# Performance work log

Measured on AMD Instinct MI355X. Metric: run time of the kernel, lower is better.

The kernel has to match this reference:

```python
import jax, jax.numpy as jnp
import numpy as np

B, T, I, H, O, L = 64, 2048, 128, 256, 1, 2


def _lstm_layer(x, w_ih, w_hh, b_ih, b_hh):
    # x: [B, T, in]; w_ih: [4H, in]; w_hh: [4H, H]; biases: [4H]
    # Batch the input-side GEMM across all timesteps (torch gate order: i, f, g, o)
    xg = jnp.einsum('bti,gi->btg', x, w_ih) + b_ih + b_hh  # [B, T, 4H]
    h0 = jnp.zeros((x.shape[0], w_hh.shape[1]), x.dtype)
    c0 = jnp.zeros_like(h0)

    def step(carry, xt):
        h, c = carry
        g = xt + h @ w_hh.T  # [B, 4H]
        i, f, gg, o = jnp.split(g, 4, axis=-1)
        i = jax.nn.sigmoid(i)
        f = jax.nn.sigmoid(f)
        gg = jnp.tanh(gg)
        o = jax.nn.sigmoid(o)
        c = f * c + i * gg
        h = o * jnp.tanh(c)
        return (h, c), h

    _, hs = jax.lax.scan(step, (h0, c0), jnp.swapaxes(xg, 0, 1))  # [T, B, H]
    return jnp.swapaxes(hs, 0, 1)  # [B, T, H]


def setup_inputs() -> dict:
    key = jax.random.key(0)
    ks = jax.random.split(key, 11)
    s_i = 1.0 / np.sqrt(H)
    return {
        'x': jax.random.normal(ks[0], (B, T, I), jnp.float32),
        'w_ih0': jax.random.uniform(ks[1], (4 * H, I), jnp.float32, -s_i, s_i),
        'w_hh0': jax.random.uniform(ks[2], (4 * H, H), jnp.float32, -s_i, s_i),
        'b_ih0': jax.random.uniform(ks[3], (4 * H,), jnp.float32, -s_i, s_i),
        'b_hh0': jax.random.uniform(ks[4], (4 * H,), jnp.float32, -s_i, s_i),
        'w_ih1': jax.random.uniform(ks[5], (4 * H, H), jnp.float32, -s_i, s_i),
        'w_hh1': jax.random.uniform(ks[6], (4 * H, H), jnp.float32, -s_i, s_i),
        'b_ih1': jax.random.uniform(ks[7], (4 * H,), jnp.float32, -s_i, s_i),
        'b_hh1': jax.random.uniform(ks[8], (4 * H,), jnp.float32, -s_i, s_i),
        'fc_w': jax.random.uniform(ks[9], (O, H), jnp.float32, -s_i, s_i),
        'fc_b': jax.random.uniform(ks[10], (O,), jnp.float32, -s_i, s_i),
    }


def reference(x, w_ih0, w_hh0, b_ih0, b_hh0, w_ih1, w_hh1, b_ih1, b_hh1, fc_w, fc_b):
    h = _lstm_layer(x, w_ih0, w_hh0, b_ih0, b_hh0)
    h = _lstm_layer(h, w_ih1, w_hh1, b_ih1, b_hh1)
    h = jax.nn.relu(h)            # relu on full sequence output (as in source)
    last = h[:, -1, :]            # [B, H]
    return last @ fc_w.T + fc_b   # [B, O]
```

## Files before the change

### kernel.cpp

```cpp
#include <hip/hip_runtime.h>

#define NT 2048
#define NI 128
#define NH 256
#define WPG 32
#define BPG 8

typedef unsigned long long u64;

__device__ __forceinline__ float sigm(float v) {
  return 1.0f / (1.0f + __expf(-v));
}
__device__ __forceinline__ float tanh_fast(float v) {
  v = fminf(fmaxf(v, -15.0f), 15.0f);
  float e = __expf(-2.0f * v);
  return (1.0f - e) / (1.0f + e);
}
__device__ __forceinline__ float lstm_act(float gi, float gf, float gg, float go,
                                          float& c) {
  const float ii = sigm(gi), ff = sigm(gf), gt = tanh_fast(gg), oo = sigm(go);
  c = ff * c + ii * gt;
  return oo * tanh_fast(c);
}

__device__ __forceinline__ int ld_flag(const int* p) {
  return __hip_atomic_load(p, __ATOMIC_RELAXED, __HIP_MEMORY_SCOPE_AGENT);
}
__device__ __forceinline__ void st_flag(int* p, int v) {
  __hip_atomic_store(p, v, __ATOMIC_RELAXED, __HIP_MEMORY_SCOPE_AGENT);
}
__device__ __forceinline__ void st_h(float* p, float v) {
  __hip_atomic_store(p, v, __ATOMIC_RELAXED, __HIP_MEMORY_SCOPE_AGENT);
}
__device__ __forceinline__ u64 ld_h64(const u64* p) {
  return __hip_atomic_load(p, __ATOMIC_RELAXED, __HIP_MEMORY_SCOPE_AGENT);
}

template <int CTRL>
__device__ __forceinline__ float dppadd(float x) {
  int s = __builtin_amdgcn_update_dpp(0, __float_as_int(x), CTRL, 0xf, 0xf, true);
  return x + __int_as_float(s);
}
__device__ __forceinline__ float red16(float v) {
  v = dppadd<0xB1>(v);
  v = dppadd<0x4E>(v);
  v = dppadd<0x141>(v);
  v = dppadd<0x140>(v);
  return v;
}

__global__ __launch_bounds__(512, 1) void lstm_persistent(
    const float* __restrict__ x,
    const float* __restrict__ wih0, const float* __restrict__ whh0,
    const float* __restrict__ bih0, const float* __restrict__ bhh0,
    const float* __restrict__ wih1, const float* __restrict__ whh1,
    const float* __restrict__ bih1, const float* __restrict__ bhh1,
    const float* __restrict__ fcw, const float* __restrict__ fcb,
    float* __restrict__ out,
    float* __restrict__ h0buf, float* __restrict__ h1buf,
    int* __restrict__ flags)
{
  extern __shared__ float sm[];
  float* zz = sm;

  const int tid = threadIdx.x;
  const int bid = blockIdx.x;
  const int g = bid & 7;
  const int j = bid >> 3;
  const int b0 = g * BPG;
  int* fA = flags + g * WPG;
  int* fB = flags + 256 + g * WPG;

  const bool isL0 = (tid < 256);
  const int lane = tid & 63;
  const int wv = (tid & 255) >> 6;
  const int ks = lane & 15;
  const int rg2 = (lane >> 4) & 1;
  const int bg = lane >> 5;
  const int u = wv * 2 + rg2;
  const int col = j * 8 + u;

  float w[4][32];
  float bs[4];
  if (isL0) {
#pragma unroll
    for (int gt = 0; gt < 4; ++gt) {
      const int R = gt * NH + col;
      bs[gt] = bih0[R] + bhh0[R];
#pragma unroll
      for (int c = 0; c < 6; ++c)
#pragma unroll
        for (int e = 0; e < 4; ++e) {
          const int k = ks * 4 + 64 * c + e;
          w[gt][c * 4 + e] = (k < NI) ? wih0[R * NI + k] : whh0[R * NH + (k - NI)];
        }
    }
  } else {
#pragma unroll
    for (int gt = 0; gt < 4; ++gt) {
      const int R = gt * NH + col;
      bs[gt] = bih1[R] + bhh1[R];
#pragma unroll
      for (int c = 0; c < 8; ++c)
#pragma unroll
        for (int e = 0; e < 4; ++e) {
          const int k = ks * 4 + 64 * c + e;
          w[gt][c * 4 + e] = (k < NH) ? wih1[R * NH + k] : whh1[R * NH + (k - NH)];
        }
    }
  }

  float cellA0 = 0.f, cellA1 = 0.f, cellB0 = 0.f, cellB1 = 0.f;
  u64 rh0 = 0, rh1 = 0;
  float4 xv = make_float4(0.f, 0.f, 0.f, 0.f);
  if (tid < 128) {
    xv = *reinterpret_cast<const float4*>(
        x + (size_t)(b0 + (tid >> 5)) * NT * NI + (tid & 31) * 4);
  }
  __syncthreads();

#pragma unroll 1
  for (int it = 0; it <= NT; ++it) {
#pragma unroll
    for (int half = 0; half < 2; ++half) {
      const int xb = half ? 4 : 0;
      int* fSelf = half ? fB : fA;
      int* fOther = half ? fA : fB;
      const int nit = half ? it + 1 : it;
      const int oxb = half ? 0 : 4;

      if (tid < 128 && it < NT)
        *reinterpret_cast<float4*>(&zz[(tid >> 5) * 640 + (tid & 31) * 4]) = xv;
      *reinterpret_cast<u64*>(&zz[(tid >> 7) * 640 + 128 + (tid & 127) * 2]) = rh0;
      *reinterpret_cast<u64*>(&zz[(tid >> 7) * 640 + 384 + (tid & 127) * 2]) = rh1;
      __syncthreads();

      if (isL0) {
        if (it < NT) {
          float acc[4][2] = {{0.f, 0.f}, {0.f, 0.f}, {0.f, 0.f}, {0.f, 0.f}};
          const float* z0 = &zz[(bg * 2 + 0) * 640 + ks * 4];
          const float* z1 = &zz[(bg * 2 + 1) * 640 + ks * 4];
#pragma unroll
          for (int c = 0; c < 6; ++c) {
            const float4 v0 = *reinterpret_cast<const float4*>(z0 + 64 * c);
            const float4 v1 = *reinterpret_cast<const float4*>(z1 + 64 * c);
#pragma unroll
            for (int gt = 0; gt < 4; ++gt) {
              acc[gt][0] = fmaf(w[gt][c * 4 + 0], v0.x, acc[gt][0]);
              acc[gt][0] = fmaf(w[gt][c * 4 + 1], v0.y, acc[gt][0]);
              acc[gt][0] = fmaf(w[gt][c * 4 + 2], v0.z, acc[gt][0]);
              acc[gt][0] = fmaf(w[gt][c * 4 + 3], v0.w, acc[gt][0]);
              acc[gt][1] = fmaf(w[gt][c * 4 + 0], v1.x, acc[gt][1]);
              acc[gt][1] = fmaf(w[gt][c * 4 + 1], v1.y, acc[gt][1]);
              acc[gt][1] = fmaf(w[gt][c * 4 + 2], v1.z, acc[gt][1]);
              acc[gt][1] = fmaf(w[gt][c * 4 + 3], v1.w, acc[gt][1]);
            }
          }
#pragma unroll
          for (int gt = 0; gt < 4; ++gt) {
            acc[gt][0] = red16(acc[gt][0]);
            acc[gt][1] = red16(acc[gt][1]);
          }
          float ca = half ? cellB0 : cellA0;
          const float ha = lstm_act(acc[0][0] + bs[0], acc[1][0] + bs[1],
                                    acc[2][0] + bs[2], acc[3][0] + bs[3], ca);
          if (half) cellB0 = ca; else cellA0 = ca;
          float cb = half ? cellB1 : cellA1;
          const float hb = lstm_act(acc[0][1] + bs[0], acc[1][1] + bs[1],
                                    acc[2][1] + bs[2], acc[3][1] + bs[3], cb);
          if (half) cellB1 = cb; else cellA1 = cb;
          if ((lane & 15) == 0) {
            const size_t base = (size_t)(it & 1) * 64;
            st_h(&h0buf[(base + (b0 + xb + bg * 2 + 0)) * NH + col], ha);
            st_h(&h0buf[(base + (b0 + xb + bg * 2 + 1)) * NH + col], hb);
          }
        }
      } else {
        if (it >= 1) {
          float acc[4][2] = {{0.f, 0.f}, {0.f, 0.f}, {0.f, 0.f}, {0.f, 0.f}};
          const float* z0 = &zz[(bg * 2 + 0) * 640 + 128 + ks * 4];
          const float* z1 = &zz[(bg * 2 + 1) * 640 + 128 + ks * 4];
#pragma unroll
          for (int c = 0; c < 8; ++c) {
            const float4 v0 = *reinterpret_cast<const float4*>(z0 + 64 * c);
            const float4 v1 = *reinterpret_cast<const float4*>(z1 + 64 * c);
#pragma unroll
            for (int gt = 0; gt < 4; ++gt) {
              acc[gt][0] = fmaf(w[gt][c * 4 + 0], v0.x, acc[gt][0]);
              acc[gt][0] = fmaf(w[gt][c * 4 + 1], v0.y, acc[gt][0]);
              acc[gt][0] = fmaf(w[gt][c * 4 + 2], v0.z, acc[gt][0]);
              acc[gt][0] = fmaf(w[gt][c * 4 + 3], v0.w, acc[gt][0]);
              acc[gt][1] = fmaf(w[gt][c * 4 + 0], v1.x, acc[gt][1]);
              acc[gt][1] = fmaf(w[gt][c * 4 + 1], v1.y, acc[gt][1]);
              acc[gt][1] = fmaf(w[gt][c * 4 + 2], v1.z, acc[gt][1]);
              acc[gt][1] = fmaf(w[gt][c * 4 + 3], v1.w, acc[gt][1]);
            }
          }
#pragma unroll
          for (int gt = 0; gt < 4; ++gt) {
            acc[gt][0] = red16(acc[gt][0]);
            acc[gt][1] = red16(acc[gt][1]);
          }
          float ca = half ? cellB0 : cellA0;
          const float ha = lstm_act(acc[0][0] + bs[0], acc[1][0] + bs[1],
                                    acc[2][0] + bs[2], acc[3][0] + bs[3], ca);
          if (half) cellB0 = ca; else cellA0 = ca;
          float cb = half ? cellB1 : cellA1;
          const float hb = lstm_act(acc[0][1] + bs[0], acc[1][1] + bs[1],
                                    acc[2][1] + bs[2], acc[3][1] + bs[3], cb);
          if (half) cellB1 = cb; else cellA1 = cb;
          if ((lane & 15) == 0) {
            const size_t base = (size_t)((it - 1) & 1) * 64;
            st_h(&h1buf[(base + (b0 + xb + bg * 2 + 0)) * NH + col], ha);
            st_h(&h1buf[(base + (b0 + xb + bg * 2 + 1)) * NH + col], hb);
          }
        }
      }

      if (tid < WPG) {
        int guard = 0;
        while (ld_flag(&fOther[tid]) < nit) {
          __builtin_amdgcn_s_sleep(1);
          if (++guard > 100000000) break;
        }
      }
      __syncthreads();

      if (nit <= NT) {
        const int p0 = (nit - 1) & 1;
        const int p1 = nit & 1;
        const int bl = tid >> 7, off = (tid & 127) * 2;
        rh0 = ld_h64(reinterpret_cast<const u64*>(
            h0buf + ((size_t)p0 * 64 + (b0 + oxb + bl)) * NH + off));
        rh1 = ld_h64(reinterpret_cast<const u64*>(
            h1buf + ((size_t)p1 * 64 + (b0 + oxb + bl)) * NH + off));
        if (tid < 128 && nit < NT) {
          xv = *reinterpret_cast<const float4*>(
              x + ((size_t)(b0 + oxb + (tid >> 5)) * NT + (size_t)nit) * NI +
              (tid & 31) * 4);
        }
      }

      if (nit <= NT) {
        if (tid < 128 && nit < NT)
          asm volatile("s_waitcnt vmcnt(3)" ::: "memory");
        else
          asm volatile("s_waitcnt vmcnt(2)" ::: "memory");
      } else {
        asm volatile("s_waitcnt vmcnt(0)" ::: "memory");
      }
      __builtin_amdgcn_s_barrier();
      if (tid == 0) st_flag(&fSelf[j], it + 1);
    }
  }

  if (j == 0) {
    if (tid < WPG) {
      int guard = 0;
      while (ld_flag(&fA[tid]) < NT + 1 || ld_flag(&fB[tid]) < NT + 1) {
        __builtin_amdgcn_s_sleep(1);
        if (++guard > 100000000) break;
      }
    }
    __syncthreads();
    const int bb = tid >> 6, ln = tid & 63;
    const float* hrow = h1buf + ((size_t)(((NT - 1) & 1)) * 64 + (b0 + bb)) * NH;
    const u64 u0 = ld_h64(reinterpret_cast<const u64*>(hrow + ln * 4));
    const u64 u1 = ld_h64(reinterpret_cast<const u64*>(hrow + ln * 4 + 2));
    const float ha = __uint_as_float((unsigned)u0);
    const float hb = __uint_as_float((unsigned)(u0 >> 32));
    const float hc = __uint_as_float((unsigned)u1);
    const float hd = __uint_as_float((unsigned)(u1 >> 32));
    const float4 w4 = *reinterpret_cast<const float4*>(fcw + ln * 4);
    float p = fmaxf(ha, 0.f) * w4.x + fmaxf(hb, 0.f) * w4.y +
              fmaxf(hc, 0.f) * w4.z + fmaxf(hd, 0.f) * w4.w;
#pragma unroll
    for (int off = 32; off >= 1; off >>= 1) p += __shfl_down(p, off, 64);
    if (ln == 0) out[b0 + bb] = p + fcb[0];
  }
}

extern "C" void kernel_launch(void* const* d_in, const int* in_sizes, int n_in,
                              void* d_out, int out_size, void* d_ws, size_t ws_size,
                              hipStream_t stream) {
  (void)in_sizes; (void)n_in; (void)out_size; (void)ws_size;
  const float* x    = (const float*)d_in[0];
  const float* wih0 = (const float*)d_in[1];
  const float* whh0 = (const float*)d_in[2];
  const float* bih0 = (const float*)d_in[3];
  const float* bhh0 = (const float*)d_in[4];
  const float* wih1 = (const float*)d_in[5];
  const float* whh1 = (const float*)d_in[6];
  const float* bih1 = (const float*)d_in[7];
  const float* bhh1 = (const float*)d_in[8];
  const float* fcw  = (const float*)d_in[9];
  const float* fcb  = (const float*)d_in[10];
  float* out = (float*)d_out;

  float* ws = (float*)d_ws;
  float* h0buf = ws;
  float* h1buf = ws + 2 * 64 * 256;
  int* flags = (int*)(ws + 4 * 64 * 256);

  const size_t zbytes = (size_t)(4 * 64 * 256) * sizeof(float) + 512 * sizeof(int);
  hipMemsetAsync(d_ws, 0, zbytes, stream);

  size_t shmem = 96 * 1024;
  if (hipFuncSetAttribute(reinterpret_cast<const void*>(lstm_persistent),
                          hipFuncAttributeMaxDynamicSharedMemorySize,
                          (int)shmem) != hipSuccess) {
    shmem = 2560 * sizeof(float);
  }

  hipLaunchKernelGGL(lstm_persistent, dim3(256), dim3(512), shmem, stream,
                     x, wih0, whh0, bih0, bhh0, wih1, whh1, bih1, bhh1,
                     fcw, fcb, out, h0buf, h1buf, flags);
}
```

Baseline: 10.74 ms.

## Restructure LSTM step sync: per-wave flag polling, gathered h stores, blocked h layout

Rewrites the per-half-step schedule of the persistent LSTM kernel. Each wave now spins on the other half's flags itself, so the extra block barrier is gone and the h/x prefetch is issued before the matvec rather than after it. Each lane computes a single batch element's activation, and the h values are gathered in shared memory. One wave then writes them as 64-bit stores and publishes the flag, using a new blocked h-buffer layout (group, column-block, batch) with padded shared rows (ZROW=644) to cut bank conflicts. This is meant to shorten the critical path of each recurrent step, at the cost of more complex indexing and a single writer wave that serialises the flag publish.

```diff
diff --git a/kernel.cpp b/kernel.cpp
--- a/kernel.cpp
+++ b/kernel.cpp
@@ -5,6 +5,7 @@
 #define NH 256
 #define WPG 32
 #define BPG 8
+#define ZROW 644
 
 typedef unsigned long long u64;
 
@@ -29,11 +30,11 @@
 __device__ __forceinline__ void st_flag(int* p, int v) {
   __hip_atomic_store(p, v, __ATOMIC_RELAXED, __HIP_MEMORY_SCOPE_AGENT);
 }
-__device__ __forceinline__ void st_h(float* p, float v) {
-  __hip_atomic_store(p, v, __ATOMIC_RELAXED, __HIP_MEMORY_SCOPE_AGENT);
-}
 __device__ __forceinline__ u64 ld_h64(const u64* p) {
   return __hip_atomic_load(p, __ATOMIC_RELAXED, __HIP_MEMORY_SCOPE_AGENT);
+}
+__device__ __forceinline__ void st_h64(u64* p, u64 v) {
+  __hip_atomic_store(p, v, __ATOMIC_RELAXED, __HIP_MEMORY_SCOPE_AGENT);
 }
 
 template <int CTRL>
@@ -61,7 +62,8 @@
     int* __restrict__ flags)
 {
   extern __shared__ float sm[];
-  float* zz = sm;
+  float* zz  = sm;
+  float* gat = sm + 4 * ZROW;
 
   const int tid = threadIdx.x;
   const int bid = blockIdx.x;
@@ -79,6 +81,8 @@
   const int bg = lane >> 5;
   const int u = wv * 2 + rg2;
   const int col = j * 8 + u;
+  const int sel = ks & 1;
+  const int myb = bg * 2 + sel;
 
   float w[4][32];
   float bs[4];
@@ -110,13 +114,20 @@
     }
   }
 
-  float cellA0 = 0.f, cellA1 = 0.f, cellB0 = 0.f, cellB1 = 0.f;
+  const int pj = tid >> 4;
+  const int pr = tid & 15;
+  const int pb = pr >> 2;
+  const int pu = pr & 3;
+  const int stage_h0 = pb * ZROW + 128 + pj * 8 + pu * 2;
+  const int stage_h1 = pb * ZROW + 384 + pj * 8 + pu * 2;
+  const int pre_base = (g * 32 + pj) * 64 + pb * 8 + pu * 2;
+  const float* xA = x + (size_t)(b0 + 0 + (tid >> 5)) * NT * NI + (tid & 31) * 4;
+  const float* xB = x + (size_t)(b0 + 4 + (tid >> 5)) * NT * NI + (tid & 31) * 4;
+
+  float cA = 0.f, cB = 0.f;
   u64 rh0 = 0, rh1 = 0;
   float4 xv = make_float4(0.f, 0.f, 0.f, 0.f);
-  if (tid < 128) {
-    xv = *reinterpret_cast<const float4*>(
-        x + (size_t)(b0 + (tid >> 5)) * NT * NI + (tid & 31) * 4);
-  }
+  if (tid < 128) xv = *reinterpret_cast<const float4*>(xA);
   __syncthreads();
 
 #pragma unroll 1
@@ -130,18 +141,39 @@
       const int oxb = half ? 0 : 4;
 
       if (tid < 128 && it < NT)
-        *reinterpret_cast<float4*>(&zz[(tid >> 5) * 640 + (tid & 31) * 4]) = xv;
-      *reinterpret_cast<u64*>(&zz[(tid >> 7) * 640 + 128 + (tid & 127) * 2]) = rh0;
-      *reinterpret_cast<u64*>(&zz[(tid >> 7) * 640 + 384 + (tid & 127) * 2]) = rh1;
+        *reinterpret_cast<float4*>(&zz[(tid >> 5) * ZROW + (tid & 31) * 4]) = xv;
+      *reinterpret_cast<u64*>(&zz[stage_h0]) = rh0;
+      *reinterpret_cast<u64*>(&zz[stage_h1]) = rh1;
       __syncthreads();
 
-      if (isL0) {
-        if (it < NT) {
-          float acc[4][2] = {{0.f, 0.f}, {0.f, 0.f}, {0.f, 0.f}, {0.f, 0.f}};
-          const float* z0 = &zz[(bg * 2 + 0) * 640 + ks * 4];
-          const float* z1 = &zz[(bg * 2 + 1) * 640 + ks * 4];
-#pragma unroll
-          for (int c = 0; c < 6; ++c) {
+      if (nit <= NT) {
+        if (lane < WPG) {
+          int guard = 0;
+          while (ld_flag(&fOther[lane]) < nit) {
+            __builtin_amdgcn_s_sleep(1);
+            if (++guard > 50000000) break;
+          }
+        }
+        asm volatile("" ::: "memory");
+        const int o0 = ((nit - 1) & 1) * 16384 + oxb * 8 + pre_base;
+        const int o1 = (nit & 1) * 16384 + oxb * 8 + pre_base;
+        rh0 = ld_h64(reinterpret_cast<const u64*>(h0buf + o0));
+        rh1 = ld_h64(reinterpret_cast<const u64*>(h1buf + o1));
+        if (tid < 128 && nit < NT) {
+          xv = *reinterpret_cast<const float4*>((half ? xA : xB) +
+                                                (size_t)nit * NI);
+        }
+      }
+
+      if (isL0 ? (it < NT) : (it >= 1)) {
+        float acc[4][2] = {{0.f, 0.f}, {0.f, 0.f}, {0.f, 0.f}, {0.f, 0.f}};
+        const int koff = isL0 ? (ks * 4) : (128 + ks * 4);
+        const float* z0 = &zz[(bg * 2 + 0) * ZROW + koff];
+        const float* z1 = &zz[(bg * 2 + 1) * ZROW + koff];
+        const int NC = isL0 ? 6 : 8;
+#pragma unroll
+        for (int c = 0; c < 8; ++c) {
+          if (c < NC) {
             const float4 v0 = *reinterpret_cast<const float4*>(z0 + 64 * c);
             const float4 v1 = *reinterpret_cast<const float4*>(z1 + 64 * c);
 #pragma unroll
@@ -156,101 +188,40 @@
               acc[gt][1] = fmaf(w[gt][c * 4 + 3], v1.w, acc[gt][1]);
             }
           }
-#pragma unroll
-          for (int gt = 0; gt < 4; ++gt) {
-            acc[gt][0] = red16(acc[gt][0]);
-            acc[gt][1] = red16(acc[gt][1]);
+        }
+        float s0[4];
+#pragma unroll
+        for (int gt = 0; gt < 4; ++gt) {
+          const float ra = red16(acc[gt][0]);
+          const float rb = red16(acc[gt][1]);
+          s0[gt] = (sel ? rb : ra) + bs[gt];
+        }
+        float c = half ? cB : cA;
+        const float h = lstm_act(s0[0], s0[1], s0[2], s0[3], c);
+        if (half) cB = c; else cA = c;
+        if (ks < 2) gat[(isL0 ? 0 : 32) + myb * 8 + u] = h;
+      }
+      asm volatile("s_waitcnt lgkmcnt(0)" ::: "memory");
+      __builtin_amdgcn_s_barrier();
+
+      if ((tid >> 6) == 1) {
+        const int l = tid & 63;
+        if (l < 32) {
+          const int layer = l >> 4, l4 = l & 15;
+          const bool ok = layer ? (it >= 1) : (it < NT);
+          if (ok) {
+            const int par = layer ? ((it - 1) & 1) : (it & 1);
+            float* hb = layer ? h1buf : h0buf;
+            const u64 v = *reinterpret_cast<const u64*>(
+                &gat[layer * 32 + (l4 >> 2) * 8 + (l4 & 3) * 2]);
+            st_h64(reinterpret_cast<u64*>(hb + par * 16384 + (g * 32 + j) * 64 +
+                                          (xb + (l4 >> 2)) * 8 + (l4 & 3) * 2),
+                   v);
           }
-          float ca = half ? cellB0 : cellA0;
-          const float ha = lstm_act(acc[0][0] + bs[0], acc[1][0] + bs[1],
-                                    acc[2][0] + bs[2], acc[3][0] + bs[3], ca);
-          if (half) cellB0 = ca; else cellA0 = ca;
-          float cb = half ? cellB1 : cellA1;
-          const float hb = lstm_act(acc[0][1] + bs[0], acc[1][1] + bs[1],
-                                    acc[2][1] + bs[2], acc[3][1] + bs[3], cb);
-          if (half) cellB1 = cb; else cellA1 = cb;
-          if ((lane & 15) == 0) {
-            const size_t base = (size_t)(it & 1) * 64;
-            st_h(&h0buf[(base + (b0 + xb + bg * 2 + 0)) * NH + col], ha);
-            st_h(&h0buf[(base + (b0 + xb + bg * 2 + 1)) * NH + col], hb);
-          }
-        }
-      } else {
-        if (it >= 1) {
-          float acc[4][2] = {{0.f, 0.f}, {0.f, 0.f}, {0.f, 0.f}, {0.f, 0.f}};
-          const float* z0 = &zz[(bg * 2 + 0) * 640 + 128 + ks * 4];
-          const float* z1 = &zz[(bg * 2 + 1) * 640 + 128 + ks * 4];
-#pragma unroll
-          for (int c = 0; c < 8; ++c) {
-            const float4 v0 = *reinterpret_cast<const float4*>(z0 + 64 * c);
-            const float4 v1 = *reinterpret_cast<const float4*>(z1 + 64 * c);
-#pragma unroll
-            for (int gt = 0; gt < 4; ++gt) {
-              acc[gt][0] = fmaf(w[gt][c * 4 + 0], v0.x, acc[gt][0]);
-              acc[gt][0] = fmaf(w[gt][c * 4 + 1], v0.y, acc[gt][0]);
-              acc[gt][0] = fmaf(w[gt][c * 4 + 2], v0.z, acc[gt][0]);
-              acc[gt][0] = fmaf(w[gt][c * 4 + 3], v0.w, acc[gt][0]);
-              acc[gt][1] = fmaf(w[gt][c * 4 + 0], v1.x, acc[gt][1]);
-              acc[gt][1] = fmaf(w[gt][c * 4 + 1], v1.y, acc[gt][1]);
-              acc[gt][1] = fmaf(w[gt][c * 4 + 2], v1.z, acc[gt][1]);
-              acc[gt][1] = fmaf(w[gt][c * 4 + 3], v1.w, acc[gt][1]);
-            }
-          }
-#pragma unroll
-          for (int gt = 0; gt < 4; ++gt) {
-            acc[gt][0] = red16(acc[gt][0]);
-            acc[gt][1] = red16(acc[gt][1]);
-          }
-          float ca = half ? cellB0 : cellA0;
-          const float ha = lstm_act(acc[0][0] + bs[0], acc[1][0] + bs[1],
-                                    acc[2][0] + bs[2], acc[3][0] + bs[3], ca);
-          if (half) cellB0 = ca; else cellA0 = ca;
-          float cb = half ? cellB1 : cellA1;
-          const float hb = lstm_act(acc[0][1] + bs[0], acc[1][1] + bs[1],
-                                    acc[2][1] + bs[2], acc[3][1] + bs[3], cb);
-          if (half) cellB1 = cb; else cellA1 = cb;
-          if ((lane & 15) == 0) {
-            const size_t base = (size_t)((it - 1) & 1) * 64;
-            st_h(&h1buf[(base + (b0 + xb + bg * 2 + 0)) * NH + col], ha);
-            st_h(&h1buf[(base + (b0 + xb + bg * 2 + 1)) * NH + col], hb);
-          }
-        }
-      }
-
-      if (tid < WPG) {
-        int guard = 0;
-        while (ld_flag(&fOther[tid]) < nit) {
-          __builtin_amdgcn_s_sleep(1);
-          if (++guard > 100000000) break;
-        }
-      }
-      __syncthreads();
-
-      if (nit <= NT) {
-        const int p0 = (nit - 1) & 1;
-        const int p1 = nit & 1;
-        const int bl = tid >> 7, off = (tid & 127) * 2;
-        rh0 = ld_h64(reinterpret_cast<const u64*>(
-            h0buf + ((size_t)p0 * 64 + (b0 + oxb + bl)) * NH + off));
-        rh1 = ld_h64(reinterpret_cast<const u64*>(
-            h1buf + ((size_t)p1 * 64 + (b0 + oxb + bl)) * NH + off));
-        if (tid < 128 && nit < NT) {
-          xv = *reinterpret_cast<const float4*>(
-              x + ((size_t)(b0 + oxb + (tid >> 5)) * NT + (size_t)nit) * NI +
-              (tid & 31) * 4);
-        }
-      }
-
-      if (nit <= NT) {
-        if (tid < 128 && nit < NT)
-          asm volatile("s_waitcnt vmcnt(3)" ::: "memory");
-        else
-          asm volatile("s_waitcnt vmcnt(2)" ::: "memory");
-      } else {
+        }
         asm volatile("s_waitcnt vmcnt(0)" ::: "memory");
-      }
-      __builtin_amdgcn_s_barrier();
-      if (tid == 0) st_flag(&fSelf[j], it + 1);
+        if ((tid & 63) == 0) st_flag(&fSelf[j], it + 1);
+      }
     }
   }
 
@@ -259,14 +230,16 @@
       int guard = 0;
       while (ld_flag(&fA[tid]) < NT + 1 || ld_flag(&fB[tid]) < NT + 1) {
         __builtin_amdgcn_s_sleep(1);
-        if (++guard > 100000000) break;
+        if (++guard > 50000000) break;
       }
     }
     __syncthreads();
     const int bb = tid >> 6, ln = tid & 63;
-    const float* hrow = h1buf + ((size_t)(((NT - 1) & 1)) * 64 + (b0 + bb)) * NH;
-    const u64 u0 = ld_h64(reinterpret_cast<const u64*>(hrow + ln * 4));
-    const u64 u1 = ld_h64(reinterpret_cast<const u64*>(hrow + ln * 4 + 2));
+    const int jj = ln >> 1, q = ln & 1;
+    const float* src = h1buf + 1 * 16384 + ((8 * 0 + g) * 0)  +
+                       ((g * 32 + jj) * 8 + bb) * 8 + q * 4;
+    const u64 u0 = ld_h64(reinterpret_cast<const u64*>(src));
+    const u64 u1 = ld_h64(reinterpret_cast<const u64*>(src + 2));
     const float ha = __uint_as_float((unsigned)u0);
     const float hb = __uint_as_float((unsigned)(u0 >> 32));
     const float hc = __uint_as_float((unsigned)u1);
@@ -299,17 +272,17 @@
 
   float* ws = (float*)d_ws;
   float* h0buf = ws;
-  float* h1buf = ws + 2 * 64 * 256;
-  int* flags = (int*)(ws + 4 * 64 * 256);
-
-  const size_t zbytes = (size_t)(4 * 64 * 256) * sizeof(float) + 512 * sizeof(int);
+  float* h1buf = ws + 32768;
+  int* flags = (int*)(ws + 65536);
+
+  const size_t zbytes = (size_t)65536 * sizeof(float) + 512 * sizeof(int);
   hipMemsetAsync(d_ws, 0, zbytes, stream);
 
   size_t shmem = 96 * 1024;
   if (hipFuncSetAttribute(reinterpret_cast<const void*>(lstm_persistent),
                           hipFuncAttributeMaxDynamicSharedMemorySize,
                           (int)shmem) != hipSuccess) {
-    shmem = 2560 * sizeof(float);
+    shmem = (4 * ZROW + 64) * sizeof(float);
   }
 
   hipLaunchKernelGGL(lstm_persistent, dim3(256), dim3(512), shmem, stream,
```

New measurement: 23.58 ms. 2.2x slower.
